# Kernel optimization log

Measured on AMD Instinct MI355X. Metric: run time of the kernel, lower is better.

The kernel has to match this reference:

```python
import jax, jax.numpy as jnp
import numpy as np

EMBED = 1024
HEADS = 16
HEAD_DIM = EMBED // HEADS


def setup_inputs() -> dict:
    key = jax.random.key(0)
    k1, k2, k3 = jax.random.split(key, 3)
    hidden_states = jax.random.normal(k1, (2, 2048, EMBED), dtype=jnp.float32)
    # Conv1D weights are stored (nx, nf): y = x @ W + b
    c_attn_w = jax.random.normal(k2, (EMBED, 3 * EMBED), dtype=jnp.float32) * 0.02
    c_attn_b = jnp.zeros((3 * EMBED,), dtype=jnp.float32)
    c_proj_w = jax.random.normal(k3, (EMBED, EMBED), dtype=jnp.float32) * 0.02
    c_proj_b = jnp.zeros((EMBED,), dtype=jnp.float32)
    return {
        "hidden_states": hidden_states,
        "c_attn_w": c_attn_w,
        "c_attn_b": c_attn_b,
        "c_proj_w": c_proj_w,
        "c_proj_b": c_proj_b,
    }


def reference(hidden_states, c_attn_w, c_attn_b, c_proj_w, c_proj_b):
    B, S, E = hidden_states.shape
    H, D = HEADS, HEAD_DIM
    fused = hidden_states @ c_attn_w + c_attn_b  # [B,S,3E]
    q, k, v = jnp.split(fused, 3, axis=-1)
    # split heads -> [B,H,S,D]
    q = q.reshape(B, S, H, D).transpose(0, 2, 1, 3)
    k = k.reshape(B, S, H, D).transpose(0, 2, 1, 3)
    v = v.reshape(B, S, H, D).transpose(0, 2, 1, 3)
    scores = jnp.einsum("bhqd,bhkd->bhqk", q, k) / jnp.sqrt(jnp.float32(D))
    probs = jax.nn.softmax(scores, axis=-1)  # NOTE: no causal mask in source
    attn = jnp.einsum("bhqk,bhkd->bhqd", probs, v)
    out = attn.transpose(0, 2, 1, 3).reshape(B, S, E)
    return out @ c_proj_w + c_proj_b
```

## Files before the change

kernel.cpp:

```cpp
#include <hip/hip_runtime.h>
#include <hip/hip_bf16.h>
#include <cstdint>
#include <cstddef>

#define E_ 1024
#define H_ 16
#define D_ 64
#define B_ 2
#define S_ 2048
#define T_ 4096
#define NQ_ 3072

typedef __bf16 bf16_t;
typedef bf16_t bf16x8 __attribute__((ext_vector_type(8)));
typedef float f32x4 __attribute__((ext_vector_type(4)));

static __device__ __forceinline__ unsigned short f2bf(float f) {
    __hip_bfloat16 h = __float2bfloat16(f);
    return __builtin_bit_cast(unsigned short, h);
}
static __device__ __forceinline__ unsigned pack2(float a, float b) {
    return (unsigned)f2bf(a) | ((unsigned)f2bf(b) << 16);
}
static __device__ __forceinline__ bf16x8 ld_frag(const unsigned short* p) {
    uint4 u = *reinterpret_cast<const uint4*>(p);
    return __builtin_bit_cast(bf16x8, u);
}
static __device__ __forceinline__ void cp16(unsigned short* lds, const unsigned short* g) {
    __builtin_amdgcn_global_load_lds(
        (const __attribute__((address_space(1))) unsigned int*)g,
        (__attribute__((address_space(3))) unsigned int*)lds, 16, 0, 0);
}
static __device__ __forceinline__ f32x4 mfma16(bf16x8 a, bf16x8 b, f32x4 c) {
    return __builtin_amdgcn_mfma_f32_16x16x32_bf16(a, b, c, 0, 0, 0);
}
static __device__ __forceinline__ unsigned pack2_trunc(unsigned a_bits, unsigned b_bits) {
    return __builtin_amdgcn_perm(b_bits, a_bits, 0x07060302u);
}


__global__ __launch_bounds__(256) void k_cvt(const float* __restrict__ in,
                                             unsigned short* __restrict__ out, int n) {
    int i = (blockIdx.x * 256 + threadIdx.x) * 4;
    if (i < n) {
        float4 v = *reinterpret_cast<const float4*>(in + i);
        int tok = i >> 10, e = i & 1023;
        size_t off = ((size_t)(tok >> 7) * 32 + (e >> 5)) * 4096 + (tok & 127) * 32 + (e & 31);
        uint2 o;
        o.x = pack2(v.x, v.y);
        o.y = pack2(v.z, v.w);
        *reinterpret_cast<uint2*>(out + off) = o;
    }
}

__global__ __launch_bounds__(256) void k_wt(const float* __restrict__ in,
                                            unsigned short* __restrict__ out, int K, int N) {
    __shared__ float t[32][33];
    int n0 = blockIdx.x * 32, k0 = blockIdx.y * 32;
    int tx = threadIdx.x, ty = threadIdx.y;
    for (int j = 0; j < 4; j++) {
        int r = ty + j * 8;
        t[r][tx] = in[(size_t)(k0 + r) * N + n0 + tx];
    }
    __syncthreads();
    int nkt = K >> 5;
    for (int j = 0; j < 4; j++) {
        int r = ty + j * 8;
        int nn = n0 + r;
        size_t off = ((size_t)(nn >> 7) * nkt + (k0 >> 5)) * 4096 + (nn & 127) * 32 + tx;
        out[off] = f2bf(t[tx][r]);
    }
}

static __device__ __forceinline__ void gemm_tile_128(
    const unsigned short* __restrict__ At,
    const unsigned short* __restrict__ Bt,
    int nkt, int m0, int n0,
    unsigned short* As, unsigned short* Bs,
    f32x4 acc[4][4])
{
    const int t = threadIdx.x;
    const int w = t >> 6, lane = t & 63, lr = lane & 15, lq = lane >> 4;
    const int wm = (w >> 1) * 64, wn = (w & 1) * 64;
    for (int mt = 0; mt < 4; mt++)
        for (int nt = 0; nt < 4; nt++)
            acc[mt][nt] = (f32x4){0.f, 0.f, 0.f, 0.f};

    const unsigned short* ag = At + (size_t)(m0 >> 7) * nkt * 4096 + t * 8;
    const unsigned short* bg = Bt + (size_t)(n0 >> 7) * nkt * 4096 + t * 8;

    for (int kt = 0; kt < nkt; kt++) {
        __syncthreads();
        cp16(&As[t * 8], ag);          cp16(&As[(t + 256) * 8], ag + 2048);
        cp16(&Bs[t * 8], bg);          cp16(&Bs[(t + 256) * 8], bg + 2048);
        ag += 4096; bg += 4096;
        __syncthreads();
        bf16x8 af[4], bfr[4];
        for (int mt = 0; mt < 4; mt++) af[mt]  = ld_frag(&As[(wm + mt * 16 + lr) * 32 + lq * 8]);
        for (int nt = 0; nt < 4; nt++) bfr[nt] = ld_frag(&Bs[(wn + nt * 16 + lr) * 32 + lq * 8]);
        for (int mt = 0; mt < 4; mt++)
            for (int nt = 0; nt < 4; nt++)
                acc[mt][nt] = mfma16(af[mt], bfr[nt], acc[mt][nt]);
    }
}

__global__ __launch_bounds__(256) void k_qkv(
    const unsigned short* __restrict__ Ab, const unsigned short* __restrict__ Wt,
    const float* __restrict__ bias,
    unsigned short* __restrict__ Qb, unsigned short* __restrict__ Kimg,
    unsigned short* __restrict__ Vimg)
{
    __shared__ __attribute__((aligned(16))) unsigned short As[128 * 32];
    __shared__ __attribute__((aligned(16))) unsigned short Bs[128 * 32];
    f32x4 acc[4][4];
    int m0 = blockIdx.x * 128, n0 = blockIdx.y * 128;
    gemm_tile_128(Ab, Wt, E_ / 32, m0, n0, As, Bs, acc);

    int t = threadIdx.x, w = t >> 6, lane = t & 63, lr = lane & 15, lq = lane >> 4;
    int wm = (w >> 1) * 64, wn = (w & 1) * 64;
    int sector = (n0 >> 10);
    for (int nt = 0; nt < 4; nt++) {
        int n = n0 + wn + nt * 16 + lr;
        float bv = bias[n];
        int nn = n & 1023, hh = nn >> 6, d = nn & 63;
        for (int mt = 0; mt < 4; mt++) {
            int tok0 = m0 + wm + mt * 16 + lq * 4;
            int bb = tok0 >> 11, s0 = tok0 & 2047;
            size_t headOff = (size_t)(bb * H_ + hh) * (S_ * D_);
            if (sector == 0) {
                for (int i = 0; i < 4; i++) {
                    float v = acc[mt][nt][i] + bv;
                    Qb[headOff + (size_t)(s0 + i) * 64 + d] = f2bf(v * 0.18033688011112042f);
                }
            } else if (sector == 1) {
                int dc = d >> 5, lq_ = (d >> 3) & 3, pos = d & 7;
                for (int i = 0; i < 4; i++) {
                    int s = s0 + i;
                    int tile = s >> 7, j = s & 127, stripe = j >> 5, jj = j & 31;
                    int h2 = (jj >> 2) & 1, slot = ((jj >> 3) << 2) | (jj & 3);
                    size_t off = headOff + (size_t)tile * 8192 +
                        ((size_t)(((stripe * 2 + h2) * 2 + dc) * 64 + lq_ * 16 + slot)) * 8 + pos;
                    Kimg[off] = f2bf(acc[mt][nt][i] + bv);
                }
            } else {
                int tile = s0 >> 7, j = s0 & 127, stripe = j >> 5, lq_ = (j >> 3) & 3, pos = j & 7;
                int dt = d >> 4;
                size_t off = headOff + (size_t)tile * 8192 +
                    ((size_t)((stripe * 4 + dt) * 64 + lq_ * 16 + (d & 15))) * 8 + pos;
                uint2 u;
                u.x = pack2(acc[mt][nt][0] + bv, acc[mt][nt][1] + bv);
                u.y = pack2(acc[mt][nt][2] + bv, acc[mt][nt][3] + bv);
                *reinterpret_cast<uint2*>(Vimg + off) = u;
            }
        }
    }
}

__global__ __launch_bounds__(256) void k_attn(
    const unsigned short* __restrict__ Qb, const unsigned short* __restrict__ Kimg,
    const unsigned short* __restrict__ Vimg, unsigned short* __restrict__ Ao)
{
    __shared__ __attribute__((aligned(16))) unsigned short smem[16896];
    unsigned short* Ks = smem;
    unsigned short* Vt = smem + 8192;
    float* Lred = (float*)(smem + 16384);
    float* Ored = (float*)smem;

    const int t = threadIdx.x, w = t >> 6, lane = t & 63, lr = lane & 15, lq = lane >> 4;

    const int id = blockIdx.x;
    const int xcd = id & 7, slot = id >> 3;
    const int qblk = slot & 31;
    const int hb = ((slot >> 5) << 3) | xcd;
    const int h = hb & 15, b = hb >> 4;

    const size_t head = (size_t)(b * H_ + h) * (S_ * D_);
    const unsigned short* Qh = Qb + head;
    const unsigned short* kg = Kimg + head + t * 8;
    const unsigned short* vg = Vimg + head + t * 8;
    const int q0 = qblk * 64;

    bf16x8 qf[4][2];
    for (int qt = 0; qt < 4; qt++)
        for (int dc = 0; dc < 2; dc++)
            qf[qt][dc] = ld_frag(&Qh[(size_t)(q0 + qt * 16 + lr) * 64 + dc * 32 + lq * 8]);

    f32x4 o[4][4];
    for (int qt = 0; qt < 4; qt++)
        for (int dt = 0; dt < 4; dt++)
            o[qt][dt] = (f32x4){0.f, 0.f, 0.f, 0.f};
    float lsum[4] = {0.f, 0.f, 0.f, 0.f};

    for (int it = 0; it < S_ / 128; it++) {
        __syncthreads();
        cp16(&Ks[t * 8], kg);                cp16(&Ks[(t + 256) * 8], kg + 2048);
        cp16(&Ks[(t + 512) * 8], kg + 4096); cp16(&Ks[(t + 768) * 8], kg + 6144);
        cp16(&Vt[t * 8], vg);                cp16(&Vt[(t + 256) * 8], vg + 2048);
        cp16(&Vt[(t + 512) * 8], vg + 4096); cp16(&Vt[(t + 768) * 8], vg + 6144);
        kg += 8192; vg += 8192;
        __syncthreads();

        f32x4 z[2][4];
#pragma unroll
        for (int h2 = 0; h2 < 2; h2++) {
            bf16x8 kf0 = ld_frag(&Ks[((w * 4 + h2 * 2 + 0) * 64 + lane) * 8]);
            bf16x8 kf1 = ld_frag(&Ks[((w * 4 + h2 * 2 + 1) * 64 + lane) * 8]);
            for (int qt = 0; qt < 4; qt++) {
                f32x4 zz = (f32x4){0.f, 0.f, 0.f, 0.f};
                zz = mfma16(kf0, qf[qt][0], zz);
                zz = mfma16(kf1, qf[qt][1], zz);
                z[h2][qt] = zz;
            }
        }
        bf16x8 pb[4];
#pragma unroll
        for (int qt = 0; qt < 4; qt++) {
            unsigned eb[8];
            float ts = 0.f;
#pragma unroll
            for (int h2 = 0; h2 < 2; h2++)
                for (int r = 0; r < 4; r++) {
                    float e = exp2f(z[h2][qt][r]);
                    unsigned ub = __builtin_bit_cast(unsigned, e);
                    eb[h2 * 4 + r] = ub;
                    ts += __builtin_bit_cast(float, ub & 0xffff0000u);
                }
            lsum[qt] += ts;
            uint4 u;
            u.x = pack2_trunc(eb[0], eb[1]);
            u.y = pack2_trunc(eb[2], eb[3]);
            u.z = pack2_trunc(eb[4], eb[5]);
            u.w = pack2_trunc(eb[6], eb[7]);
            pb[qt] = __builtin_bit_cast(bf16x8, u);
        }
        bf16x8 vf[4];
#pragma unroll
        for (int dt = 0; dt < 4; dt++)
            vf[dt] = ld_frag(&Vt[((w * 4 + dt) * 64 + lane) * 8]);
        for (int qt = 0; qt < 4; qt++)
            for (int dt = 0; dt < 4; dt++)
                o[qt][dt] = mfma16(vf[dt], pb[qt], o[qt][dt]);
    }

    __syncthreads();

    for (int qt = 0; qt < 4; qt++) {
        lsum[qt] += __shfl_xor(lsum[qt], 16, 64);
        lsum[qt] += __shfl_xor(lsum[qt], 32, 64);
    }
    if (lq == 0)
        for (int qt = 0; qt < 4; qt++)
            Lred[w * 64 + qt * 16 + lr] = lsum[qt];

    for (int ww = 0; ww < 4; ww++) {
        if (w == ww) {
            for (int qt = 0; qt < 4; qt++)
                for (int dt = 0; dt < 4; dt++) {
                    int q = qt * 16 + lr, d = dt * 16 + lq * 4;
                    float4* p = reinterpret_cast<float4*>(&Ored[q * 68 + d]);
                    float4 vv = {o[qt][dt][0], o[qt][dt][1], o[qt][dt][2], o[qt][dt][3]};
                    if (ww == 0) *p = vv;
                    else {
                        float4 c = *p;
                        c.x += vv.x; c.y += vv.y; c.z += vv.z; c.w += vv.w;
                        *p = c;
                    }
                }
        }
        __syncthreads();
    }

    {
        int q = t >> 2, dsg = (t & 3) * 16;
        float inv = 1.0f / (Lred[q] + Lred[64 + q] + Lred[128 + q] + Lred[192 + q]);
        const float* rp = &Ored[q * 68 + dsg];
        unsigned u[8];
        for (int j = 0; j < 8; j++)
            u[j] = pack2(rp[2 * j] * inv, rp[2 * j + 1] * inv);
        int tok = b * S_ + q0 + q, e = h * 64 + dsg;
        size_t off = ((size_t)(tok >> 7) * 32 + (e >> 5)) * 4096 + (tok & 127) * 32 + (e & 31);
        uint4 s0 = {u[0], u[1], u[2], u[3]};
        uint4 s1 = {u[4], u[5], u[6], u[7]};
        *reinterpret_cast<uint4*>(&Ao[off]) = s0;
        *reinterpret_cast<uint4*>(&Ao[off + 8]) = s1;
    }
}

__global__ __launch_bounds__(256) void k_proj(
    const unsigned short* __restrict__ Ab, const unsigned short* __restrict__ Wt,
    const float* __restrict__ bias, float* __restrict__ out)
{
    __shared__ __attribute__((aligned(16))) unsigned short As[128 * 32];
    __shared__ __attribute__((aligned(16))) unsigned short Bs[128 * 32];
    f32x4 acc[4][4];
    int m0 = blockIdx.x * 128, n0 = blockIdx.y * 128;
    gemm_tile_128(Ab, Wt, E_ / 32, m0, n0, As, Bs, acc);

    int t = threadIdx.x, w = t >> 6, lane = t & 63, lr = lane & 15, lq = lane >> 4;
    int wm = (w >> 1) * 64, wn = (w & 1) * 64;
    for (int nt = 0; nt < 4; nt++) {
        int n = n0 + wn + nt * 16 + lr;
        float bv = bias[n];
        for (int mt = 0; mt < 4; mt++)
            for (int i = 0; i < 4; i++) {
                int tok = m0 + wm + mt * 16 + lq * 4 + i;
                out[(size_t)tok * E_ + n] = acc[mt][nt][i] + bv;
            }
    }
}

extern "C" void kernel_launch(void* const* d_in, const int* in_sizes, int n_in,
                              void* d_out, int out_size, void* d_ws, size_t ws_size,
                              hipStream_t stream) {
    const float* hs = (const float*)d_in[0];
    const float* w1 = (const float*)d_in[1];
    const float* b1 = (const float*)d_in[2];
    const float* w2 = (const float*)d_in[3];
    const float* b2 = (const float*)d_in[4];
    float* out = (float*)d_out;

    char* ws = (char*)d_ws;
    unsigned short* hb  = (unsigned short*)(ws);
    unsigned short* w1t = (unsigned short*)(ws + (size_t)( 8 << 20));
    unsigned short* w2t = (unsigned short*)(ws + (size_t)(14 << 20));
    unsigned short* Qb  = (unsigned short*)(ws + (size_t)(16 << 20));
    unsigned short* Kim = (unsigned short*)(ws + (size_t)(24 << 20));
    unsigned short* Vim = (unsigned short*)(ws + (size_t)(32 << 20));
    unsigned short* Ao  = (unsigned short*)(ws + (size_t)(40 << 20));

    k_cvt<<<dim3(T_ * E_ / 1024), dim3(256), 0, stream>>>(hs, hb, T_ * E_);
    k_wt<<<dim3(NQ_ / 32, E_ / 32), dim3(32, 8), 0, stream>>>(w1, w1t, E_, NQ_);
    k_wt<<<dim3(E_ / 32, E_ / 32), dim3(32, 8), 0, stream>>>(w2, w2t, E_, E_);
    k_qkv<<<dim3(T_ / 128, NQ_ / 128), dim3(256), 0, stream>>>(hb, w1t, b1, Qb, Kim, Vim);
    k_attn<<<dim3(S_ / 64 * H_ * B_), dim3(256), 0, stream>>>(Qb, Kim, Vim, Ao);
    k_proj<<<dim3(T_ / 128, E_ / 128), dim3(256), 0, stream>>>(Ao, w2t, b2, out);
}
```

Measured before the change: 224.4 us.

## Transpose MFMA operands for vectorized GEMM epilogues and compute softmax sums via MFMA

The GEMM tile helper gains a template flag that swaps the MFMA operands, so each lane's accumulator holds four consecutive output columns instead of four rows. The Q, K and projection epilogues then write uint2 or float4 vectors in place of scattered scalar stores. In attention, the per-row exp sum is now produced by an MFMA against a vector of ones rather than scalar adds plus cross-lane shuffles, and exp2f is replaced with the hardware intrinsic. This cuts store transactions and VALU work, at the cost of a few extra MFMA instructions per tile.

```diff
diff --git a/kernel.cpp b/kernel.cpp
--- a/kernel.cpp
+++ b/kernel.cpp
@@ -72,6 +72,7 @@
     }
 }
 
+template <bool TR>
 static __device__ __forceinline__ void gemm_tile_128(
     const unsigned short* __restrict__ At,
     const unsigned short* __restrict__ Bt,
@@ -100,7 +101,8 @@
         for (int nt = 0; nt < 4; nt++) bfr[nt] = ld_frag(&Bs[(wn + nt * 16 + lr) * 32 + lq * 8]);
         for (int mt = 0; mt < 4; mt++)
             for (int nt = 0; nt < 4; nt++)
-                acc[mt][nt] = mfma16(af[mt], bfr[nt], acc[mt][nt]);
+                acc[mt][nt] = TR ? mfma16(bfr[nt], af[mt], acc[mt][nt])
+                                 : mfma16(af[mt], bfr[nt], acc[mt][nt]);
     }
 }
 
@@ -114,35 +116,22 @@
     __shared__ __attribute__((aligned(16))) unsigned short Bs[128 * 32];
     f32x4 acc[4][4];
     int m0 = blockIdx.x * 128, n0 = blockIdx.y * 128;
-    gemm_tile_128(Ab, Wt, E_ / 32, m0, n0, As, Bs, acc);
+    int sector = (n0 >> 10);
+    if (sector == 2) gemm_tile_128<false>(Ab, Wt, E_ / 32, m0, n0, As, Bs, acc);
+    else             gemm_tile_128<true >(Ab, Wt, E_ / 32, m0, n0, As, Bs, acc);
 
     int t = threadIdx.x, w = t >> 6, lane = t & 63, lr = lane & 15, lq = lane >> 4;
     int wm = (w >> 1) * 64, wn = (w & 1) * 64;
-    int sector = (n0 >> 10);
-    for (int nt = 0; nt < 4; nt++) {
-        int n = n0 + wn + nt * 16 + lr;
-        float bv = bias[n];
-        int nn = n & 1023, hh = nn >> 6, d = nn & 63;
-        for (int mt = 0; mt < 4; mt++) {
-            int tok0 = m0 + wm + mt * 16 + lq * 4;
-            int bb = tok0 >> 11, s0 = tok0 & 2047;
-            size_t headOff = (size_t)(bb * H_ + hh) * (S_ * D_);
-            if (sector == 0) {
-                for (int i = 0; i < 4; i++) {
-                    float v = acc[mt][nt][i] + bv;
-                    Qb[headOff + (size_t)(s0 + i) * 64 + d] = f2bf(v * 0.18033688011112042f);
-                }
-            } else if (sector == 1) {
-                int dc = d >> 5, lq_ = (d >> 3) & 3, pos = d & 7;
-                for (int i = 0; i < 4; i++) {
-                    int s = s0 + i;
-                    int tile = s >> 7, j = s & 127, stripe = j >> 5, jj = j & 31;
-                    int h2 = (jj >> 2) & 1, slot = ((jj >> 3) << 2) | (jj & 3);
-                    size_t off = headOff + (size_t)tile * 8192 +
-                        ((size_t)(((stripe * 2 + h2) * 2 + dc) * 64 + lq_ * 16 + slot)) * 8 + pos;
-                    Kimg[off] = f2bf(acc[mt][nt][i] + bv);
-                }
-            } else {
+
+    if (sector == 2) {
+        for (int nt = 0; nt < 4; nt++) {
+            int n = n0 + wn + nt * 16 + lr;
+            float bv = bias[n];
+            int nn = n & 1023, hh = nn >> 6, d = nn & 63;
+            for (int mt = 0; mt < 4; mt++) {
+                int tok0 = m0 + wm + mt * 16 + lq * 4;
+                int bb = tok0 >> 11, s0 = tok0 & 2047;
+                size_t headOff = (size_t)(bb * H_ + hh) * (S_ * D_);
                 int tile = s0 >> 7, j = s0 & 127, stripe = j >> 5, lq_ = (j >> 3) & 3, pos = j & 7;
                 int dt = d >> 4;
                 size_t off = headOff + (size_t)tile * 8192 +
@@ -153,6 +142,36 @@
                 *reinterpret_cast<uint2*>(Vimg + off) = u;
             }
         }
+    } else {
+        for (int nt = 0; nt < 4; nt++) {
+            int n = n0 + wn + nt * 16 + lq * 4;
+            float4 bv4 = *reinterpret_cast<const float4*>(&bias[n]);
+            int nn = n & 1023, hh = nn >> 6, d0 = nn & 63;
+            for (int mt = 0; mt < 4; mt++) {
+                int tok = m0 + wm + mt * 16 + lr;
+                int bb = tok >> 11, s = tok & 2047;
+                size_t headOff = (size_t)(bb * H_ + hh) * (S_ * D_);
+                float v0 = acc[mt][nt][0] + bv4.x, v1 = acc[mt][nt][1] + bv4.y;
+                float v2 = acc[mt][nt][2] + bv4.z, v3 = acc[mt][nt][3] + bv4.w;
+                if (sector == 0) {
+                    const float c = 0.18033688011112042f;
+                    uint2 u;
+                    u.x = pack2(v0 * c, v1 * c);
+                    u.y = pack2(v2 * c, v3 * c);
+                    *reinterpret_cast<uint2*>(Qb + headOff + (size_t)s * 64 + d0) = u;
+                } else {
+                    int dc = d0 >> 5, lq_ = (d0 >> 3) & 3, pos = d0 & 7;
+                    int tile = s >> 7, j = s & 127, stripe = j >> 5, jj = j & 31;
+                    int h2 = (jj >> 2) & 1, slot = ((jj >> 3) << 2) | (jj & 3);
+                    size_t off = headOff + (size_t)tile * 8192 +
+                        ((size_t)(((stripe * 2 + h2) * 2 + dc) * 64 + lq_ * 16 + slot)) * 8 + pos;
+                    uint2 u;
+                    u.x = pack2(v0, v1);
+                    u.y = pack2(v2, v3);
+                    *reinterpret_cast<uint2*>(Kimg + off) = u;
+                }
+            }
+        }
     }
 }
 
@@ -185,11 +204,19 @@
         for (int dc = 0; dc < 2; dc++)
             qf[qt][dc] = ld_frag(&Qh[(size_t)(q0 + qt * 16 + lr) * 64 + dc * 32 + lq * 8]);
 
+    bf16x8 ones;
+    {
+        uint4 u = {0x3f803f80u, 0x3f803f80u, 0x3f803f80u, 0x3f803f80u};
+        ones = __builtin_bit_cast(bf16x8, u);
+    }
+
     f32x4 o[4][4];
-    for (int qt = 0; qt < 4; qt++)
+    f32x4 oL[4];
+    for (int qt = 0; qt < 4; qt++) {
+        oL[qt] = (f32x4){0.f, 0.f, 0.f, 0.f};
         for (int dt = 0; dt < 4; dt++)
             o[qt][dt] = (f32x4){0.f, 0.f, 0.f, 0.f};
-    float lsum[4] = {0.f, 0.f, 0.f, 0.f};
+    }
 
     for (int it = 0; it < S_ / 128; it++) {
         __syncthreads();
@@ -215,24 +242,23 @@
         bf16x8 pb[4];
 #pragma unroll
         for (int qt = 0; qt < 4; qt++) {
-            unsigned eb[8];
-            float ts = 0.f;
-#pragma unroll
-            for (int h2 = 0; h2 < 2; h2++)
-                for (int r = 0; r < 4; r++) {
-                    float e = exp2f(z[h2][qt][r]);
-                    unsigned ub = __builtin_bit_cast(unsigned, e);
-                    eb[h2 * 4 + r] = ub;
-                    ts += __builtin_bit_cast(float, ub & 0xffff0000u);
-                }
-            lsum[qt] += ts;
+            unsigned e0 = __builtin_bit_cast(unsigned, __builtin_amdgcn_exp2f(z[0][qt][0]));
+            unsigned e1 = __builtin_bit_cast(unsigned, __builtin_amdgcn_exp2f(z[0][qt][1]));
+            unsigned e2 = __builtin_bit_cast(unsigned, __builtin_amdgcn_exp2f(z[0][qt][2]));
+            unsigned e3 = __builtin_bit_cast(unsigned, __builtin_amdgcn_exp2f(z[0][qt][3]));
+            unsigned e4 = __builtin_bit_cast(unsigned, __builtin_amdgcn_exp2f(z[1][qt][0]));
+            unsigned e5 = __builtin_bit_cast(unsigned, __builtin_amdgcn_exp2f(z[1][qt][1]));
+            unsigned e6 = __builtin_bit_cast(unsigned, __builtin_amdgcn_exp2f(z[1][qt][2]));
+            unsigned e7 = __builtin_bit_cast(unsigned, __builtin_amdgcn_exp2f(z[1][qt][3]));
             uint4 u;
-            u.x = pack2_trunc(eb[0], eb[1]);
-            u.y = pack2_trunc(eb[2], eb[3]);
-            u.z = pack2_trunc(eb[4], eb[5]);
-            u.w = pack2_trunc(eb[6], eb[7]);
+            u.x = pack2_trunc(e0, e1);
+            u.y = pack2_trunc(e2, e3);
+            u.z = pack2_trunc(e4, e5);
+            u.w = pack2_trunc(e6, e7);
             pb[qt] = __builtin_bit_cast(bf16x8, u);
         }
+        for (int qt = 0; qt < 4; qt++)
+            oL[qt] = mfma16(ones, pb[qt], oL[qt]);
         bf16x8 vf[4];
 #pragma unroll
         for (int dt = 0; dt < 4; dt++)
@@ -244,13 +270,9 @@
 
     __syncthreads();
 
-    for (int qt = 0; qt < 4; qt++) {
-        lsum[qt] += __shfl_xor(lsum[qt], 16, 64);
-        lsum[qt] += __shfl_xor(lsum[qt], 32, 64);
-    }
     if (lq == 0)
         for (int qt = 0; qt < 4; qt++)
-            Lred[w * 64 + qt * 16 + lr] = lsum[qt];
+            Lred[w * 64 + qt * 16 + lr] = oL[qt][0];
 
     for (int ww = 0; ww < 4; ww++) {
         if (w == ww) {
@@ -294,18 +316,19 @@
     __shared__ __attribute__((aligned(16))) unsigned short Bs[128 * 32];
     f32x4 acc[4][4];
     int m0 = blockIdx.x * 128, n0 = blockIdx.y * 128;
-    gemm_tile_128(Ab, Wt, E_ / 32, m0, n0, As, Bs, acc);
+    gemm_tile_128<true>(Ab, Wt, E_ / 32, m0, n0, As, Bs, acc);
 
     int t = threadIdx.x, w = t >> 6, lane = t & 63, lr = lane & 15, lq = lane >> 4;
     int wm = (w >> 1) * 64, wn = (w & 1) * 64;
     for (int nt = 0; nt < 4; nt++) {
-        int n = n0 + wn + nt * 16 + lr;
-        float bv = bias[n];
-        for (int mt = 0; mt < 4; mt++)
-            for (int i = 0; i < 4; i++) {
-                int tok = m0 + wm + mt * 16 + lq * 4 + i;
-                out[(size_t)tok * E_ + n] = acc[mt][nt][i] + bv;
-            }
+        int n = n0 + wn + nt * 16 + lq * 4;
+        float4 bv4 = *reinterpret_cast<const float4*>(&bias[n]);
+        for (int mt = 0; mt < 4; mt++) {
+            int tok = m0 + wm + mt * 16 + lr;
+            float4 vv = {acc[mt][nt][0] + bv4.x, acc[mt][nt][1] + bv4.y,
+                         acc[mt][nt][2] + bv4.z, acc[mt][nt][3] + bv4.w};
+            *reinterpret_cast<float4*>(&out[(size_t)tok * E_ + n]) = vv;
+        }
     }
 }
 
```

After: 218.6 us. -2.6%, faster.
